# Optimization experiments

Hardware: AMD Instinct MI355X
Metric: run time of the kernel (lower is better)

The kernel has to match this reference:

```python
import jax, jax.numpy as jnp
import numpy as np

B, C, H, W = 4, 512, 64, 64
RED = 2
IC = C // RED  # inter_channels = 256


def _conv1x1(x, w, b):
    # mmcv ConvModule default: conv(+bias) then ReLU
    return jax.nn.relu(jnp.einsum('bchw,oc->bohw', x, w) + b[None, :, None, None])


def setup_inputs() -> dict:
    key = jax.random.key(0)
    ks = jax.random.split(key, 9)
    s_q = 0.02  # small init so exp(-dist) stays in a sane range
    return {
        'features': jax.random.normal(ks[0], (B, C, H, W), jnp.float32),
        'qw': jax.random.normal(ks[1], (IC, C), jnp.float32) * s_q,
        'qb': jnp.zeros((IC,), jnp.float32),
        'kw': jax.random.normal(ks[2], (IC, C), jnp.float32) * s_q,
        'kb': jnp.zeros((IC,), jnp.float32),
        'vw': jax.random.normal(ks[3], (C, C), jnp.float32) * s_q,
        'vb': jnp.zeros((C,), jnp.float32),
        'cw': jax.random.normal(ks[4], (IC, 2), jnp.float32) * s_q,
        'cb': jnp.zeros((IC,), jnp.float32),
    }


def reference(features, qw, qb, kw, kb, vw, vb, cw, cb):
    b, c, h, w = features.shape
    q = _conv1x1(features, qw, qb)   # [b, IC, h, w]
    k = _conv1x1(features, kw, kb)   # [b, IC, h, w]
    v = _conv1x1(features, vw, vb)   # [b, C,  h, w]

    # coordinate grid: channel 0 varies along w, channel 1 along h
    lin = jnp.linspace(-1.0, 1.0, h)
    A = jnp.broadcast_to(lin[None, :], (h, w))
    coord = jnp.broadcast_to(jnp.stack([A, A.T], axis=0)[None], (b, 2, h, w))
    cc = _conv1x1(coord, cw, cb)     # [b, IC, h, w]

    q = q + cc
    k = k + cc

    n = h * w
    Qf = q.reshape(b, -1, n).transpose(0, 2, 1)  # [b, n, IC]
    Kf = k.reshape(b, -1, n)                     # [b, IC, n]

    dots = jnp.einsum('bnc,bcm->bnm', Qf, Kf)    # [b, n, n]
    a_sq = jnp.sum(Qf * Qf, axis=-1)             # [b, n]
    b_sq = jnp.sum(Kf * Kf, axis=1)              # [b, n]
    D = a_sq[:, :, None] + b_sq[:, None, :] - 2.0 * dots
    S = jnp.exp(-D)
    S = S / (jnp.sum(S, axis=-1, keepdims=True) + 1e-14)

    Vf = v.reshape(b, c, n)                      # [b, C, n]
    out = jnp.einsum('bcn,bnm->bcm', Vf, S).reshape(b, c, h, w)
    return out + features
```

## Files before the change

kernel.cpp:

```cpp
#include <hip/hip_runtime.h>
#include <math.h>

#define BATCH 4
#define CH    512
#define ICH   256
#define NPIX  4096

typedef short short8 __attribute__((ext_vector_type(8)));
typedef float floatx4 __attribute__((ext_vector_type(4)));

#define BK   64
#define TS   136

static __device__ __forceinline__ unsigned short f2bf(float x) {
    union { float f; unsigned u; } v; v.f = x;
    unsigned r = (v.u + 0x7FFF + ((v.u >> 16) & 1)) >> 16;
    return (unsigned short)r;
}
static __device__ __forceinline__ float bf2f(unsigned short u) {
    union { unsigned u; float f; } v; v.u = ((unsigned)u) << 16; return v.f;
}
static __device__ __forceinline__ unsigned pack_bf(unsigned ue, unsigned uo) {
    return ((ue + 0x8000u) >> 16) | ((uo + 0x8000u) & 0xFFFF0000u);
}

static __device__ __forceinline__ void gld16(const unsigned short* g, unsigned short* l) {
    __builtin_amdgcn_global_load_lds(
        (const __attribute__((address_space(1))) unsigned int*)g,
        (__attribute__((address_space(3))) unsigned int*)l,
        16, 0, 0);
}

#define STAGE_TILE(L, M, row0, RS, k0)                                        \
    {                                                                         \
        int r_  = (it*32) + wid*8 + (lane >> 3);                              \
        int c_  = (lane & 7) ^ ((lane >> 3) & 7);                             \
        gld16(&M[(size_t)((row0) + r_)*(RS) + (k0) + c_*8],                   \
              &L[(it*32 + wid*8)*64]);                                        \
    }

#define STG64(L, M, row0, RS, k0, u)                                          \
    {                                                                         \
        int r_  = (u)*64 + wid*8 + (lane >> 3);                               \
        int c_  = (lane & 7) ^ ((lane >> 3) & 7);                             \
        gld16(&M[(size_t)((row0) + r_)*(RS) + (k0) + c_*8],                   \
              &L[((u)*64 + wid*8)*64]);                                       \
    }

#define FRAG(L, row, ks) \
    (*(const short8*)&L[(row)*64 + (((((ks)<<2) + quad) ^ (lo & 7)) << 3)])

__global__ __launch_bounds__(256)
void prep_w(const float* __restrict__ qw, const float* __restrict__ kw,
            const float* __restrict__ vw, unsigned short* __restrict__ Wb)
{
    int i = (blockIdx.x*256 + threadIdx.x) * 4;
    const float* src;
    int off;
    if (i < 256*512)            { src = qw; off = i; }
    else if (i < 512*512)       { src = kw; off = i - 256*512; }
    else                        { src = vw; off = i - 512*512; }
    float4 f = *(const float4*)&src[off];
    unsigned short pk[4] = { f2bf(f.x), f2bf(f.y), f2bf(f.z), f2bf(f.w) };
    *(uint2*)&Wb[i] = *(uint2*)pk;
}

__global__ __launch_bounds__(256)
void prep_ft(const float* __restrict__ feat, unsigned short* __restrict__ Ft)
{
    __shared__ unsigned short S[64][65];
    const int t = threadIdx.x;
    const int n0 = blockIdx.x * 64, c0 = blockIdx.y * 64, b = blockIdx.z;

    #pragma unroll
    for (int rep = 0; rep < 4; rep++) {
        int cl = rep*16 + (t >> 4), col4 = (t & 15) * 4;
        float4 f = *(const float4*)&feat[((size_t)b*CH + c0 + cl)*NPIX + n0 + col4];
        S[cl][col4 + 0] = f2bf(f.x);
        S[cl][col4 + 1] = f2bf(f.y);
        S[cl][col4 + 2] = f2bf(f.z);
        S[cl][col4 + 3] = f2bf(f.w);
    }
    __syncthreads();
    #pragma unroll
    for (int rep = 0; rep < 4; rep++) {
        int nn = rep*16 + (t >> 4), cq = t & 15;
        unsigned short h4[4];
        #pragma unroll
        for (int j = 0; j < 4; j++) h4[j] = S[cq*4 + j][nn];
        *(uint2*)&Ft[((size_t)b*NPIX + n0 + nn)*CH + c0 + cq*4] = *(uint2*)h4;
    }
}

__global__ __launch_bounds__(256)
void conv_mfma(const unsigned short* __restrict__ Ft,
               const unsigned short* __restrict__ Wb,
               const float* __restrict__ qb, const float* __restrict__ kb,
               const float* __restrict__ vb,
               const float* __restrict__ cw, const float* __restrict__ cb,
               unsigned short* __restrict__ Qt, unsigned short* __restrict__ Kt,
               unsigned short* __restrict__ Vt)
{
    __shared__ unsigned short SH[128*TS];
    unsigned short* L0 = SH;
    unsigned short* L2 = SH + 128*64;

    const int tid = threadIdx.x;
    const int wid = tid >> 6, lane = tid & 63, quad = lane >> 4, lo = lane & 15;
    const int n0 = blockIdx.x * 128;
    const int yb = blockIdx.y;
    const int bz = blockIdx.z;
    const int o_base = yb * 128;
    const int waveA = (wid >> 1) * 64, waveB = (wid & 1) * 64;
    const int is_v = (yb >= 4);
    const size_t fb = (size_t)bz*NPIX;

    floatx4 acc[4][4] = {};

    for (int k0 = 0; k0 < CH; k0 += BK) {
        #pragma unroll
        for (int it = 0; it < 4; it++) {
            STAGE_TILE(L0, Ft, fb + n0, CH, k0);
            STAGE_TILE(L2, Wb, o_base,  CH, k0);
        }
        __syncthreads();
        if (!is_v) {
            #pragma unroll
            for (int ks = 0; ks < 2; ks++) {
                short8 af[4], bw[4];
                #pragma unroll
                for (int i = 0; i < 4; i++) af[i] = FRAG(L0, waveA + i*16 + lo, ks);
                #pragma unroll
                for (int j = 0; j < 4; j++) bw[j] = FRAG(L2, waveB + j*16 + lo, ks);
                #pragma unroll
                for (int i = 0; i < 4; i++)
                    #pragma unroll
                    for (int j = 0; j < 4; j++)
                        acc[i][j] = __builtin_amdgcn_mfma_f32_16x16x32_bf16(af[i], bw[j], acc[i][j], 0, 0, 0);
            }
        } else {
            #pragma unroll
            for (int ks = 0; ks < 2; ks++) {
                short8 aw[4], bf[4];
                #pragma unroll
                for (int i = 0; i < 4; i++) aw[i] = FRAG(L2, waveA + i*16 + lo, ks);
                #pragma unroll
                for (int j = 0; j < 4; j++) bf[j] = FRAG(L0, waveB + j*16 + lo, ks);
                #pragma unroll
                for (int i = 0; i < 4; i++)
                    #pragma unroll
                    for (int j = 0; j < 4; j++)
                        acc[i][j] = __builtin_amdgcn_mfma_f32_16x16x32_bf16(aw[i], bf[j], acc[i][j], 0, 0, 0);
            }
        }
        __syncthreads();
    }

    const float step = 2.0f / 63.0f;
    if (!is_v) {
        const float* bp = (yb < 2) ? qb : kb;
        const int icg0 = (yb & 1) * 128;
        #pragma unroll
        for (int ib = 0; ib < 4; ib++) {
            int colL = waveB + ib*16 + lo;
            int ic = icg0 + colL;
            float bias = bp[ic];
            float cw0 = cw[ic*2+0], cw1 = cw[ic*2+1], cbv = cb[ic];
            #pragma unroll
            for (int ia = 0; ia < 4; ia++) {
                int rowL = waveA + ia*16 + quad*4;
                #pragma unroll
                for (int r = 0; r < 4; r++) {
                    int n = n0 + rowL + r;
                    float cx = -1.f + (n & 63)*step;
                    float cy = -1.f + (n >> 6)*step;
                    float v = fmaxf(acc[ia][ib][r] + bias, 0.f)
                            + fmaxf(cw0*cx + cw1*cy + cbv, 0.f);
                    unsigned u = __float_as_uint(v);
                    unsigned p = __shfl_xor(u, 1, 64);
                    if ((lo & 1) == 0)
                        *(unsigned*)&SH[(rowL + r)*TS + colL] = pack_bf(u, p);
                }
            }
        }
    } else {
        const int c_blk0 = (yb - 4) * 128;
        #pragma unroll
        for (int ia = 0; ia < 4; ia++) {
            int rowL = waveA + ia*16 + quad*4;
            #pragma unroll
            for (int r = 0; r < 4; r++) {
                float bias = vb[c_blk0 + rowL + r];
                #pragma unroll
                for (int ib = 0; ib < 4; ib++) {
                    int colL = waveB + ib*16 + lo;
                    float v = fmaxf(acc[ia][ib][r] + bias, 0.f);
                    unsigned u = __float_as_uint(v);
                    unsigned p = __shfl_xor(u, 1, 64);
                    if ((lo & 1) == 0)
                        *(unsigned*)&SH[(rowL + r)*TS + colL] = pack_bf(u, p);
                }
            }
        }
    }
    __syncthreads();

    unsigned short* dstp;
    int row0, rs, col0;
    if (!is_v) { dstp = ((yb < 2) ? Qt : Kt) + (size_t)bz*NPIX*ICH;
                 row0 = n0; rs = ICH; col0 = (yb & 1) * 128; }
    else       { dstp = Vt + (size_t)bz*CH*NPIX;
                 row0 = (yb - 4) * 128; rs = NPIX; col0 = n0; }
    #pragma unroll
    for (int it = 0; it < 8; it++) {
        int f = it*256 + tid;
        int row = f >> 4, col = (f & 15) * 8;
        uint4 v = *(const uint4*)&SH[row*TS + col];
        *(uint4*)&dstp[(size_t)(row0 + row)*rs + col0 + col] = v;
    }
}

__global__ __launch_bounds__(256)
void sqb_kernel(const unsigned short* __restrict__ Qt,
                const unsigned short* __restrict__ Kt,
                float* __restrict__ asq, float* __restrict__ bsq)
{
    int n = blockIdx.x*256 + threadIdx.x;
    int b = blockIdx.y;
    const unsigned short* q = Qt + ((size_t)b*NPIX + n)*ICH;
    const unsigned short* k = Kt + ((size_t)b*NPIX + n)*ICH;
    float qs = 0.f, ks = 0.f;
    #pragma unroll 4
    for (int i = 0; i < ICH/8; i++) {
        uint4 v = *(const uint4*)&q[i*8];
        const unsigned short* s = (const unsigned short*)&v;
        #pragma unroll
        for (int j = 0; j < 8; j++) { float a = bf2f(s[j]); qs += a*a; }
        uint4 w = *(const uint4*)&k[i*8];
        const unsigned short* t = (const unsigned short*)&w;
        #pragma unroll
        for (int j = 0; j < 8; j++) { float a = bf2f(t[j]); ks += a*a; }
    }
    asq[b*NPIX + n] = qs;
    bsq[b*NPIX + n] = ks;
}

__global__ __launch_bounds__(256)
void dots_mfma(const unsigned short* __restrict__ Kt_,
               const unsigned short* __restrict__ Qt_,
               const float* __restrict__ asq_, const float* __restrict__ bsq_,
               unsigned short* __restrict__ St_, float* __restrict__ rsum_,
               int b0)
{
    __shared__ unsigned short SH[128*TS];
    unsigned short* Al = SH;
    unsigned short* Bl = SH + 128*64;

    const int tid = threadIdx.x;
    const int wid = tid >> 6, lane = tid & 63, quad = lane >> 4, lo = lane & 15;
    const int m0 = blockIdx.x * 128, n0 = blockIdx.y * 128;
    const int bz = blockIdx.z, gb = b0 + bz;
    const int waveM = (wid >> 1) * 64, waveN = (wid & 1) * 64;

    const unsigned short* Kt = Kt_ + (size_t)gb*NPIX*ICH;
    const unsigned short* Qt = Qt_ + (size_t)gb*NPIX*ICH;
    const float* asq = asq_ + (size_t)gb*NPIX;
    const float* bsq = bsq_ + (size_t)gb*NPIX;
    unsigned short* St = St_ + (size_t)bz*NPIX*NPIX;
    float* rsum = rsum_ + (size_t)gb*NPIX;

    floatx4 acc[4][4] = {};

    for (int k0 = 0; k0 < ICH; k0 += BK) {
        #pragma unroll
        for (int it = 0; it < 4; it++) {
            STAGE_TILE(Al, Kt, m0, ICH, k0);
            STAGE_TILE(Bl, Qt, n0, ICH, k0);
        }
        __syncthreads();
        #pragma unroll
        for (int ks = 0; ks < 2; ks++) {
            short8 a[4], bfr[4];
            #pragma unroll
            for (int im = 0; im < 4; im++) a[im]  = FRAG(Al, waveM + im*16 + lo, ks);
            #pragma unroll
            for (int in = 0; in < 4; in++) bfr[in] = FRAG(Bl, waveN + in*16 + lo, ks);
            #pragma unroll
            for (int im = 0; im < 4; im++)
                #pragma unroll
                for (int in = 0; in < 4; in++)
                    acc[im][in] = __builtin_amdgcn_mfma_f32_16x16x32_bf16(
                        a[im], bfr[in], acc[im][in], 0, 0, 0);
        }
        __syncthreads();
    }

    #pragma unroll
    for (int in = 0; in < 4; in++) {
        int nl = waveN + in*16 + lo;
        float aq = asq[n0 + nl];
        float colsum = 0.f;
        #pragma unroll
        for (int im = 0; im < 4; im++) {
            int mb = waveM + im*16 + quad*4;
            #pragma unroll
            for (int r = 0; r < 4; r++) {
                float d = aq + bsq[m0 + mb + r] - 2.f*acc[im][in][r];
                float s = __expf(-d);
                colsum += s;
                unsigned u = __float_as_uint(s);
                unsigned p = __shfl_xor(u, 1, 64);
                if ((lo & 1) == 0)
                    *(unsigned*)&SH[(mb + r)*TS + nl] = pack_bf(u, p);
            }
        }
        colsum += __shfl_xor(colsum, 16, 64);
        colsum += __shfl_xor(colsum, 32, 64);
        if (quad == 0) atomicAdd(&rsum[n0 + nl], colsum);
    }
    __syncthreads();

    #pragma unroll
    for (int it = 0; it < 8; it++) {
        int f = it*256 + tid;
        int row = f >> 4, col = (f & 15) * 8;
        uint4 v = *(const uint4*)&SH[row*TS + col];
        *(uint4*)&St[(size_t)(m0 + row)*NPIX + n0 + col] = v;
    }
}

__global__ __launch_bounds__(256)
void vscale_kernel(const unsigned short* __restrict__ Vt,
                   const float* __restrict__ rsum,
                   unsigned short* __restrict__ Vp, int b0)
{
    int gb = b0 + blockIdx.y;
    size_t base = (size_t)gb*CH*NPIX + ((size_t)blockIdx.x*256 + threadIdx.x) * 8;
    int n = (int)(base & (NPIX - 1));
    const float* rs = rsum + (size_t)gb*NPIX;
    uint4 v = *(const uint4*)&Vt[base];
    const unsigned short* s = (const unsigned short*)&v;
    unsigned short pk[8];
    #pragma unroll
    for (int i = 0; i < 8; i++)
        pk[i] = f2bf(bf2f(s[i]) / (rs[n + i] + 1e-14f));
    *(uint4*)&Vp[base] = *(uint4*)pk;
}

#define PVBUF 24576
#define PVNT  (NPIX/BK)

__global__ __launch_bounds__(512)
void pv_mfma(const unsigned short* __restrict__ Vp_,
             const unsigned short* __restrict__ St_,
             const float* __restrict__ feat_, float* __restrict__ out_,
             int b0)
{
    __shared__ unsigned short SH3[3*PVBUF];
    const int tid = threadIdx.x;
    const int wid = tid >> 6, lane = tid & 63, quad = lane >> 4, lo = lane & 15;
    const int wm = wid >> 2;
    const int wn = wid & 3;
    const int m0 = blockIdx.x * 256, c0 = blockIdx.y * 128;
    const int bz = blockIdx.z, gb = b0 + bz;

    const unsigned short* Vp = Vp_ + (size_t)gb*CH*NPIX;
    const unsigned short* St = St_ + (size_t)bz*NPIX*NPIX;
    const float* feat = feat_ + (size_t)gb*CH*NPIX;
    float* out = out_ + (size_t)gb*CH*NPIX;

    floatx4 acc[4][4] = {};

    {
        unsigned short* A0 = SH3;            unsigned short* B0 = SH3 + 128*64;
        unsigned short* A1 = SH3 + PVBUF;    unsigned short* B1 = A1  + 128*64;
        STG64(A0, Vp, c0, NPIX, 0, 0);  STG64(A0, Vp, c0, NPIX, 0, 1);
        STG64(B0, St, m0, NPIX, 0, 0);  STG64(B0, St, m0, NPIX, 0, 1);
        STG64(B0, St, m0, NPIX, 0, 2);  STG64(B0, St, m0, NPIX, 0, 3);
        STG64(A1, Vp, c0, NPIX, BK, 0); STG64(A1, Vp, c0, NPIX, BK, 1);
        STG64(B1, St, m0, NPIX, BK, 0); STG64(B1, St, m0, NPIX, BK, 1);
        STG64(B1, St, m0, NPIX, BK, 2); STG64(B1, St, m0, NPIX, BK, 3);
    }
    asm volatile("s_waitcnt vmcnt(6)" ::: "memory");
    __builtin_amdgcn_s_barrier();

    int pc = 0, pn = 2;
    for (int s = 0; s < PVNT; ++s) {
        unsigned short* Ac = SH3 + pc*PVBUF;
        unsigned short* Bc = Ac + 128*64;
        unsigned short* An = SH3 + pn*PVBUF;
        unsigned short* Bn = An + 128*64;
        const int k2 = (s + 2) * BK;
        const bool stg = (s < PVNT - 2);

        short8 a0[2][4], b01[2][2];
        #pragma unroll
        for (int ks = 0; ks < 2; ks++) {
            #pragma unroll
            for (int i = 0; i < 4; i++)
                a0[ks][i] = FRAG(Ac, wm*64 + i*16 + lo, ks);
            #pragma unroll
            for (int j = 0; j < 2; j++)
                b01[ks][j] = FRAG(Bc, wn*64 + j*16 + lo, ks);
        }
        if (stg) {
            STG64(An, Vp, c0, NPIX, k2, 0);
            STG64(An, Vp, c0, NPIX, k2, 1);
            STG64(Bn, St, m0, NPIX, k2, 0);
        }
        __builtin_amdgcn_s_barrier();
        __builtin_amdgcn_s_setprio(1);
        #pragma unroll
        for (int ks = 0; ks < 2; ks++)
            #pragma unroll
            for (int i = 0; i < 4; i++)
                #pragma unroll
                for (int j = 0; j < 2; j++)
                    acc[i][j] = __builtin_amdgcn_mfma_f32_16x16x32_bf16(
                        a0[ks][i], b01[ks][j], acc[i][j], 0, 0, 0);
        __builtin_amdgcn_s_setprio(0);
        __builtin_amdgcn_s_barrier();

        short8 b23[2][2];
        #pragma unroll
        for (int ks = 0; ks < 2; ks++)
            #pragma unroll
            for (int j = 0; j < 2; j++)
                b23[ks][j] = FRAG(Bc, wn*64 + (j+2)*16 + lo, ks);
        if (stg) {
            STG64(Bn, St, m0, NPIX, k2, 1);
            STG64(Bn, St, m0, NPIX, k2, 2);
            STG64(Bn, St, m0, NPIX, k2, 3);
        }
        __builtin_amdgcn_s_barrier();
        __builtin_amdgcn_s_setprio(1);
        #pragma unroll
        for (int ks = 0; ks < 2; ks++)
            #pragma unroll
            for (int i = 0; i < 4; i++)
                #pragma unroll
                for (int j = 0; j < 2; j++)
                    acc[i][j+2] = __builtin_amdgcn_mfma_f32_16x16x32_bf16(
                        a0[ks][i], b23[ks][j], acc[i][j+2], 0, 0, 0);
        __builtin_amdgcn_s_setprio(0);

        if (s < PVNT - 2)       asm volatile("s_waitcnt vmcnt(6)" ::: "memory");
        else if (s == PVNT - 2) asm volatile("s_waitcnt vmcnt(0)" ::: "memory");
        __builtin_amdgcn_s_barrier();

        pc = (pc == 2) ? 0 : pc + 1;
        pn = (pn == 2) ? 0 : pn + 1;
    }

    #pragma unroll
    for (int i = 0; i < 4; i++) {
        int cr = c0 + wm*64 + i*16 + quad*4;
        #pragma unroll
        for (int r = 0; r < 4; r++) {
            size_t rowbase = (size_t)(cr + r)*NPIX;
            #pragma unroll
            for (int j = 0; j < 4; j++) {
                int m = m0 + wn*64 + j*16 + lo;
                out[rowbase + m] = acc[i][j][r] + feat[rowbase + m];
            }
        }
    }
}

extern "C" void kernel_launch(void* const* d_in, const int* in_sizes, int n_in,
                              void* d_out, int out_size, void* d_ws, size_t ws_size,
                              hipStream_t stream)
{
    const float* feat = (const float*)d_in[0];
    const float* qw   = (const float*)d_in[1];
    const float* qb   = (const float*)d_in[2];
    const float* kw   = (const float*)d_in[3];
    const float* kb   = (const float*)d_in[4];
    const float* vw   = (const float*)d_in[5];
    const float* vb   = (const float*)d_in[6];
    const float* cw   = (const float*)d_in[7];
    const float* cb   = (const float*)d_in[8];
    float* out = (float*)d_out;
    char* ws = (char*)d_ws;
    char* ws0 = ws;

    unsigned short* Ft  = (unsigned short*)ws;  ws += (size_t)BATCH*NPIX*CH*2;
    unsigned short* Wb  = (unsigned short*)ws;  ws += (size_t)1024*CH*2;
    unsigned short* Qt  = (unsigned short*)ws;  ws += (size_t)BATCH*NPIX*ICH*2;
    unsigned short* Kt  = (unsigned short*)ws;  ws += (size_t)BATCH*NPIX*ICH*2;
    unsigned short* Vt  = (unsigned short*)ws;  ws += (size_t)BATCH*CH*NPIX*2;
    unsigned short* Vp  = (unsigned short*)ws;  ws += (size_t)BATCH*CH*NPIX*2;
    float*         asq  = (float*)ws;           ws += (size_t)BATCH*NPIX*4;
    float*         bsq  = (float*)ws;           ws += (size_t)BATCH*NPIX*4;
    float*         rsum = (float*)ws;           ws += (size_t)BATCH*NPIX*4;
    unsigned short* St  = (unsigned short*)ws;

    const size_t st1 = (size_t)NPIX*NPIX*2;
    const size_t fixed = (size_t)(ws - ws0);
    const int nb = (ws_size >= fixed + (size_t)BATCH*st1) ? BATCH : 1;

    hipMemsetAsync(rsum, 0, (size_t)BATCH*NPIX*sizeof(float), stream);

    prep_w<<<dim3(512), 256, 0, stream>>>(qw, kw, vw, Wb);
    prep_ft<<<dim3(NPIX/64, CH/64, BATCH), 256, 0, stream>>>(feat, Ft);

    conv_mfma<<<dim3(NPIX/128, 8, BATCH), 256, 0, stream>>>(
        Ft, Wb, qb, kb, vb, cw, cb, Qt, Kt, Vt);

    sqb_kernel<<<dim3(NPIX/256, BATCH), 256, 0, stream>>>(Qt, Kt, asq, bsq);

    for (int b0 = 0; b0 < BATCH; b0 += nb) {
        dots_mfma<<<dim3(NPIX/128, NPIX/128, nb), 256, 0, stream>>>(
            Kt, Qt, asq, bsq, St, rsum, b0);
        vscale_kernel<<<dim3(CH*NPIX/(256*8), nb), 256, 0, stream>>>(
            Vt, rsum, Vp, b0);
        pv_mfma<<<dim3(NPIX/256, CH/128, nb), 512, 0, stream>>>(
            Vp, St, feat, out, b0);
    }
}
```

Before: 306.3 us.

## Double-buffer LDS tiles in conv and dots GEMMs with MFMA priority hints

Converts the single-buffered K loops in conv_mfma and dots_mfma into double-buffered pipelines. The next K-slice is issued into the alternate LDS buffer via global_load_lds while MFMAs run on the current one, leaving one barrier per iteration. It also raises wave priority around the MFMA blocks. LDS per block grows from about 34KB to 64KB, which may cut occupancy, and correctness depends on the async load/barrier ordering.

```diff
diff --git a/kernel.cpp b/kernel.cpp
--- a/kernel.cpp
+++ b/kernel.cpp
@@ -35,20 +35,20 @@
     {                                                                         \
         int r_  = (it*32) + wid*8 + (lane >> 3);                              \
         int c_  = (lane & 7) ^ ((lane >> 3) & 7);                             \
-        gld16(&M[(size_t)((row0) + r_)*(RS) + (k0) + c_*8],                   \
-              &L[(it*32 + wid*8)*64]);                                        \
+        gld16(&(M)[(size_t)((row0) + r_)*(RS) + (k0) + c_*8],                 \
+              &(L)[(it*32 + wid*8)*64]);                                      \
     }
 
 #define STG64(L, M, row0, RS, k0, u)                                          \
     {                                                                         \
         int r_  = (u)*64 + wid*8 + (lane >> 3);                               \
         int c_  = (lane & 7) ^ ((lane >> 3) & 7);                             \
-        gld16(&M[(size_t)((row0) + r_)*(RS) + (k0) + c_*8],                   \
-              &L[((u)*64 + wid*8)*64]);                                       \
+        gld16(&(M)[(size_t)((row0) + r_)*(RS) + (k0) + c_*8],                 \
+              &(L)[((u)*64 + wid*8)*64]);                                     \
     }
 
 #define FRAG(L, row, ks) \
-    (*(const short8*)&L[(row)*64 + (((((ks)<<2) + quad) ^ (lo & 7)) << 3)])
+    (*(const short8*)&(L)[(row)*64 + (((((ks)<<2) + quad) ^ (lo & 7)) << 3)])
 
 __global__ __launch_bounds__(256)
 void prep_w(const float* __restrict__ qw, const float* __restrict__ kw,
@@ -92,6 +92,8 @@
     }
 }
 
+#define CBUF 16384
+
 __global__ __launch_bounds__(256)
 void conv_mfma(const unsigned short* __restrict__ Ft,
                const unsigned short* __restrict__ Wb,
@@ -101,9 +103,7 @@
                unsigned short* __restrict__ Qt, unsigned short* __restrict__ Kt,
                unsigned short* __restrict__ Vt)
 {
-    __shared__ unsigned short SH[128*TS];
-    unsigned short* L0 = SH;
-    unsigned short* L2 = SH + 128*64;
+    __shared__ unsigned short SH[2*CBUF];
 
     const int tid = threadIdx.x;
     const int wid = tid >> 6, lane = tid & 63, quad = lane >> 4, lo = lane & 15;
@@ -117,13 +117,31 @@
 
     floatx4 acc[4][4] = {};
 
-    for (int k0 = 0; k0 < CH; k0 += BK) {
+    {
+        unsigned short* P0 = SH;
+        unsigned short* P2 = SH + 8192;
         #pragma unroll
         for (int it = 0; it < 4; it++) {
-            STAGE_TILE(L0, Ft, fb + n0, CH, k0);
-            STAGE_TILE(L2, Wb, o_base,  CH, k0);
-        }
-        __syncthreads();
+            STAGE_TILE(P0, Ft, fb + n0, CH, 0);
+            STAGE_TILE(P2, Wb, o_base,  CH, 0);
+        }
+    }
+    __syncthreads();
+
+    #pragma unroll
+    for (int s = 0; s < 8; ++s) {
+        unsigned short* L0 = SH + (s & 1)*CBUF;
+        unsigned short* L2 = L0 + 8192;
+        if (s < 7) {
+            unsigned short* N0 = SH + ((s + 1) & 1)*CBUF;
+            unsigned short* N2 = N0 + 8192;
+            const int k0 = (s + 1)*BK;
+            #pragma unroll
+            for (int it = 0; it < 4; it++) {
+                STAGE_TILE(N0, Ft, fb + n0, CH, k0);
+                STAGE_TILE(N2, Wb, o_base,  CH, k0);
+            }
+        }
         if (!is_v) {
             #pragma unroll
             for (int ks = 0; ks < 2; ks++) {
@@ -132,11 +150,13 @@
                 for (int i = 0; i < 4; i++) af[i] = FRAG(L0, waveA + i*16 + lo, ks);
                 #pragma unroll
                 for (int j = 0; j < 4; j++) bw[j] = FRAG(L2, waveB + j*16 + lo, ks);
+                __builtin_amdgcn_s_setprio(1);
                 #pragma unroll
                 for (int i = 0; i < 4; i++)
                     #pragma unroll
                     for (int j = 0; j < 4; j++)
                         acc[i][j] = __builtin_amdgcn_mfma_f32_16x16x32_bf16(af[i], bw[j], acc[i][j], 0, 0, 0);
+                __builtin_amdgcn_s_setprio(0);
             }
         } else {
             #pragma unroll
@@ -146,11 +166,13 @@
                 for (int i = 0; i < 4; i++) aw[i] = FRAG(L2, waveA + i*16 + lo, ks);
                 #pragma unroll
                 for (int j = 0; j < 4; j++) bf[j] = FRAG(L0, waveB + j*16 + lo, ks);
+                __builtin_amdgcn_s_setprio(1);
                 #pragma unroll
                 for (int i = 0; i < 4; i++)
                     #pragma unroll
                     for (int j = 0; j < 4; j++)
                         acc[i][j] = __builtin_amdgcn_mfma_f32_16x16x32_bf16(aw[i], bf[j], acc[i][j], 0, 0, 0);
+                __builtin_amdgcn_s_setprio(0);
             }
         }
         __syncthreads();
@@ -252,9 +274,7 @@
                unsigned short* __restrict__ St_, float* __restrict__ rsum_,
                int b0)
 {
-    __shared__ unsigned short SH[128*TS];
-    unsigned short* Al = SH;
-    unsigned short* Bl = SH + 128*64;
+    __shared__ unsigned short SH[2*CBUF];
 
     const int tid = threadIdx.x;
     const int wid = tid >> 6, lane = tid & 63, quad = lane >> 4, lo = lane & 15;
@@ -271,13 +291,31 @@
 
     floatx4 acc[4][4] = {};
 
-    for (int k0 = 0; k0 < ICH; k0 += BK) {
+    {
+        unsigned short* P0 = SH;
+        unsigned short* P2 = SH + 8192;
         #pragma unroll
         for (int it = 0; it < 4; it++) {
-            STAGE_TILE(Al, Kt, m0, ICH, k0);
-            STAGE_TILE(Bl, Qt, n0, ICH, k0);
-        }
-        __syncthreads();
+            STAGE_TILE(P0, Kt, m0, ICH, 0);
+            STAGE_TILE(P2, Qt, n0, ICH, 0);
+        }
+    }
+    __syncthreads();
+
+    #pragma unroll
+    for (int s = 0; s < 4; ++s) {
+        unsigned short* Al = SH + (s & 1)*CBUF;
+        unsigned short* Bl = Al + 8192;
+        if (s < 3) {
+            unsigned short* An = SH + ((s + 1) & 1)*CBUF;
+            unsigned short* Bn = An + 8192;
+            const int k0 = (s + 1)*BK;
+            #pragma unroll
+            for (int it = 0; it < 4; it++) {
+                STAGE_TILE(An, Kt, m0, ICH, k0);
+                STAGE_TILE(Bn, Qt, n0, ICH, k0);
+            }
+        }
         #pragma unroll
         for (int ks = 0; ks < 2; ks++) {
             short8 a[4], bfr[4];
@@ -285,12 +323,14 @@
             for (int im = 0; im < 4; im++) a[im]  = FRAG(Al, waveM + im*16 + lo, ks);
             #pragma unroll
             for (int in = 0; in < 4; in++) bfr[in] = FRAG(Bl, waveN + in*16 + lo, ks);
+            __builtin_amdgcn_s_setprio(1);
             #pragma unroll
             for (int im = 0; im < 4; im++)
                 #pragma unroll
                 for (int in = 0; in < 4; in++)
                     acc[im][in] = __builtin_amdgcn_mfma_f32_16x16x32_bf16(
                         a[im], bfr[in], acc[im][in], 0, 0, 0);
+            __builtin_amdgcn_s_setprio(0);
         }
         __syncthreads();
     }
```

Measured after the change: 320.8 us. 4.7% more time.

## Pipeline dots kernel with triple-buffered LDS and a larger 128x256 tile

Applied to the files above, without the earlier changes.

Restructures the distance/exp kernel to use 512 threads and a 128x256 output tile per block, raising reuse of the K tile. Global-to-LDS loads go through a three-stage ring buffer, with prefetch two K-steps ahead interleaved between MFMA halves and explicit vmcnt waits plus raw barriers. s_setprio is raised around the MFMA bursts. This aims to hide load latency and cut per-block overhead, but it uses more LDS (about 144KB) and registers, which lowers occupancy, and the hand-placed waitcnt and barriers make correctness fragile.

```diff
diff --git a/kernel.cpp b/kernel.cpp
--- a/kernel.cpp
+++ b/kernel.cpp
@@ -11,6 +11,7 @@
 
 #define BK   64
 #define TS   136
+#define TS2  264
 
 static __device__ __forceinline__ unsigned short f2bf(float x) {
     union { float f; unsigned u; } v; v.f = x;
@@ -35,20 +36,20 @@
     {                                                                         \
         int r_  = (it*32) + wid*8 + (lane >> 3);                              \
         int c_  = (lane & 7) ^ ((lane >> 3) & 7);                             \
-        gld16(&M[(size_t)((row0) + r_)*(RS) + (k0) + c_*8],                   \
-              &L[(it*32 + wid*8)*64]);                                        \
+        gld16(&(M)[(size_t)((row0) + r_)*(RS) + (k0) + c_*8],                 \
+              &(L)[(it*32 + wid*8)*64]);                                      \
     }
 
 #define STG64(L, M, row0, RS, k0, u)                                          \
     {                                                                         \
         int r_  = (u)*64 + wid*8 + (lane >> 3);                               \
         int c_  = (lane & 7) ^ ((lane >> 3) & 7);                             \
-        gld16(&M[(size_t)((row0) + r_)*(RS) + (k0) + c_*8],                   \
-              &L[((u)*64 + wid*8)*64]);                                       \
+        gld16(&(M)[(size_t)((row0) + r_)*(RS) + (k0) + c_*8],                 \
+              &(L)[((u)*64 + wid*8)*64]);                                     \
     }
 
 #define FRAG(L, row, ks) \
-    (*(const short8*)&L[(row)*64 + (((((ks)<<2) + quad) ^ (lo & 7)) << 3)])
+    (*(const short8*)&(L)[(row)*64 + (((((ks)<<2) + quad) ^ (lo & 7)) << 3)])
 
 __global__ __launch_bounds__(256)
 void prep_w(const float* __restrict__ qw, const float* __restrict__ kw,
@@ -245,22 +246,23 @@
     bsq[b*NPIX + n] = ks;
 }
 
-__global__ __launch_bounds__(256)
+#define DBUF 24576
+#define DNT  (ICH/BK)
+
+__global__ __launch_bounds__(512)
 void dots_mfma(const unsigned short* __restrict__ Kt_,
                const unsigned short* __restrict__ Qt_,
                const float* __restrict__ asq_, const float* __restrict__ bsq_,
                unsigned short* __restrict__ St_, float* __restrict__ rsum_,
                int b0)
 {
-    __shared__ unsigned short SH[128*TS];
-    unsigned short* Al = SH;
-    unsigned short* Bl = SH + 128*64;
-
+    __shared__ unsigned short SH3[3*DBUF];
     const int tid = threadIdx.x;
     const int wid = tid >> 6, lane = tid & 63, quad = lane >> 4, lo = lane & 15;
-    const int m0 = blockIdx.x * 128, n0 = blockIdx.y * 128;
+    const int wm = wid >> 2;
+    const int wn = wid & 3;
+    const int m0 = blockIdx.x * 128, n0 = blockIdx.y * 256;
     const int bz = blockIdx.z, gb = b0 + bz;
-    const int waveM = (wid >> 1) * 64, waveN = (wid & 1) * 64;
 
     const unsigned short* Kt = Kt_ + (size_t)gb*NPIX*ICH;
     const unsigned short* Qt = Qt_ + (size_t)gb*NPIX*ICH;
@@ -271,47 +273,105 @@
 
     floatx4 acc[4][4] = {};
 
-    for (int k0 = 0; k0 < ICH; k0 += BK) {
-        #pragma unroll
-        for (int it = 0; it < 4; it++) {
-            STAGE_TILE(Al, Kt, m0, ICH, k0);
-            STAGE_TILE(Bl, Qt, n0, ICH, k0);
-        }
-        __syncthreads();
+    {
+        unsigned short* A0 = SH3;            unsigned short* B0 = SH3 + 128*64;
+        unsigned short* A1 = SH3 + DBUF;     unsigned short* B1 = A1  + 128*64;
+        STG64(A0, Kt, m0, ICH, 0, 0);  STG64(A0, Kt, m0, ICH, 0, 1);
+        STG64(B0, Qt, n0, ICH, 0, 0);  STG64(B0, Qt, n0, ICH, 0, 1);
+        STG64(B0, Qt, n0, ICH, 0, 2);  STG64(B0, Qt, n0, ICH, 0, 3);
+        STG64(A1, Kt, m0, ICH, BK, 0); STG64(A1, Kt, m0, ICH, BK, 1);
+        STG64(B1, Qt, n0, ICH, BK, 0); STG64(B1, Qt, n0, ICH, BK, 1);
+        STG64(B1, Qt, n0, ICH, BK, 2); STG64(B1, Qt, n0, ICH, BK, 3);
+    }
+    asm volatile("s_waitcnt vmcnt(6)" ::: "memory");
+    __builtin_amdgcn_s_barrier();
+
+    int pc = 0, pn = 2;
+    #pragma unroll
+    for (int s = 0; s < DNT; ++s) {
+        unsigned short* Ac = SH3 + pc*DBUF;
+        unsigned short* Bc = Ac + 128*64;
+        unsigned short* An = SH3 + pn*DBUF;
+        unsigned short* Bn = An + 128*64;
+        const int k2 = (s + 2) * BK;
+        const bool stg = (s < DNT - 2);
+
+        short8 a0[2][4], b01[2][2];
         #pragma unroll
         for (int ks = 0; ks < 2; ks++) {
-            short8 a[4], bfr[4];
-            #pragma unroll
-            for (int im = 0; im < 4; im++) a[im]  = FRAG(Al, waveM + im*16 + lo, ks);
-            #pragma unroll
-            for (int in = 0; in < 4; in++) bfr[in] = FRAG(Bl, waveN + in*16 + lo, ks);
-            #pragma unroll
-            for (int im = 0; im < 4; im++)
-                #pragma unroll
-                for (int in = 0; in < 4; in++)
-                    acc[im][in] = __builtin_amdgcn_mfma_f32_16x16x32_bf16(
-                        a[im], bfr[in], acc[im][in], 0, 0, 0);
-        }
-        __syncthreads();
-    }
-
-    #pragma unroll
-    for (int in = 0; in < 4; in++) {
-        int nl = waveN + in*16 + lo;
+            #pragma unroll
+            for (int i = 0; i < 4; i++)
+                a0[ks][i] = FRAG(Ac, wm*64 + i*16 + lo, ks);
+            #pragma unroll
+            for (int j = 0; j < 2; j++)
+                b01[ks][j] = FRAG(Bc, wn*64 + j*16 + lo, ks);
+        }
+        if (stg) {
+            STG64(An, Kt, m0, ICH, k2, 0);
+            STG64(An, Kt, m0, ICH, k2, 1);
+            STG64(Bn, Qt, n0, ICH, k2, 0);
+        }
+        __builtin_amdgcn_s_barrier();
+        __builtin_amdgcn_s_setprio(1);
+        #pragma unroll
+        for (int ks = 0; ks < 2; ks++)
+            #pragma unroll
+            for (int i = 0; i < 4; i++)
+                #pragma unroll
+                for (int j = 0; j < 2; j++)
+                    acc[i][j] = __builtin_amdgcn_mfma_f32_16x16x32_bf16(
+                        a0[ks][i], b01[ks][j], acc[i][j], 0, 0, 0);
+        __builtin_amdgcn_s_setprio(0);
+        __builtin_amdgcn_s_barrier();
+
+        short8 b23[2][2];
+        #pragma unroll
+        for (int ks = 0; ks < 2; ks++)
+            #pragma unroll
+            for (int j = 0; j < 2; j++)
+                b23[ks][j] = FRAG(Bc, wn*64 + (j+2)*16 + lo, ks);
+        if (stg) {
+            STG64(Bn, Qt, n0, ICH, k2, 1);
+            STG64(Bn, Qt, n0, ICH, k2, 2);
+            STG64(Bn, Qt, n0, ICH, k2, 3);
+        }
+        __builtin_amdgcn_s_barrier();
+        __builtin_amdgcn_s_setprio(1);
+        #pragma unroll
+        for (int ks = 0; ks < 2; ks++)
+            #pragma unroll
+            for (int i = 0; i < 4; i++)
+                #pragma unroll
+                for (int j = 0; j < 2; j++)
+                    acc[i][j+2] = __builtin_amdgcn_mfma_f32_16x16x32_bf16(
+                        a0[ks][i], b23[ks][j], acc[i][j+2], 0, 0, 0);
+        __builtin_amdgcn_s_setprio(0);
+
+        if (s < DNT - 2)       asm volatile("s_waitcnt vmcnt(6)" ::: "memory");
+        else if (s == DNT - 2) asm volatile("s_waitcnt vmcnt(0)" ::: "memory");
+        __builtin_amdgcn_s_barrier();
+
+        pc = (pc == 2) ? 0 : pc + 1;
+        pn = (pn == 2) ? 0 : pn + 1;
+    }
+
+    #pragma unroll
+    for (int j = 0; j < 4; j++) {
+        int nl = wn*64 + j*16 + lo;
         float aq = asq[n0 + nl];
         float colsum = 0.f;
         #pragma unroll
-        for (int im = 0; im < 4; im++) {
-            int mb = waveM + im*16 + quad*4;
+        for (int i = 0; i < 4; i++) {
+            int mb = wm*64 + i*16 + quad*4;
             #pragma unroll
             for (int r = 0; r < 4; r++) {
-                float d = aq + bsq[m0 + mb + r] - 2.f*acc[im][in][r];
-                float s = __expf(-d);
-                colsum += s;
-                unsigned u = __float_as_uint(s);
+                float d = aq + bsq[m0 + mb + r] - 2.f*acc[i][j][r];
+                float sv = __expf(-d);
+                colsum += sv;
+                unsigned u = __float_as_uint(sv);
                 unsigned p = __shfl_xor(u, 1, 64);
                 if ((lo & 1) == 0)
-                    *(unsigned*)&SH[(mb + r)*TS + nl] = pack_bf(u, p);
+                    *(unsigned*)&SH3[(mb + r)*TS2 + nl] = pack_bf(u, p);
             }
         }
         colsum += __shfl_xor(colsum, 16, 64);
@@ -322,9 +382,9 @@
 
     #pragma unroll
     for (int it = 0; it < 8; it++) {
-        int f = it*256 + tid;
-        int row = f >> 4, col = (f & 15) * 8;
-        uint4 v = *(const uint4*)&SH[row*TS + col];
+        int f = it*512 + tid;
+        int row = f >> 5, col = (f & 31) * 8;
+        uint4 v = *(const uint4*)&SH3[row*TS2 + col];
         *(uint4*)&St[(size_t)(m0 + row)*NPIX + n0 + col] = v;
     }
 }
@@ -510,7 +570,7 @@
     sqb_kernel<<<dim3(NPIX/256, BATCH), 256, 0, stream>>>(Qt, Kt, asq, bsq);
 
     for (int b0 = 0; b0 < BATCH; b0 += nb) {
-        dots_mfma<<<dim3(NPIX/128, NPIX/128, nb), 256, 0, stream>>>(
+        dots_mfma<<<dim3(NPIX/128, NPIX/256, nb), 512, 0, stream>>>(
             Kt, Qt, asq, bsq, St, rsum, b0);
         vscale_kernel<<<dim3(CH*NPIX/(256*8), nb), 256, 0, stream>>>(
             Vt, rsum, Vp, b0);
```

New measurement: 328.9 us. +7.4%, slower.
